# Kernel optimization log

Measured on AMD Instinct MI355X. Metric: run time of the kernel, lower is better.

The kernel has to match this reference:

```python
import jax, jax.numpy as jnp
import numpy as np

C = 192

def _dw_conv(x, w, k):
    # x: [B, C, H, W]; w: [C, 1, k, k]; depthwise => feature_group_count=C
    pad = k // 2
    return jax.lax.conv_general_dilated(
        x, w,
        window_strides=(1, 1),
        padding=[(pad, pad), (pad, pad)],
        dimension_numbers=("NCHW", "OIHW", "NCHW"),
        feature_group_count=x.shape[1],
    )

def setup_inputs() -> dict:
    key = jax.random.key(0)
    k1, k2, k3 = jax.random.split(key, 3)
    x = jax.random.normal(k1, (32, C, 64, 64), dtype=jnp.float32)
    # depthwise kernels: (out_ch=C, in_ch/groups=1, kh, kw), fan_in-style scaling
    w5 = jax.random.normal(k2, (C, 1, 5, 5), dtype=jnp.float32) * (1.0 / 5.0)
    w51 = jax.random.normal(k3, (C, 1, 51, 51), dtype=jnp.float32) * (1.0 / 51.0)
    return {"x": x, "w5": w5, "w51": w51}

def reference(x, w5, w51):
    # out = dw5(x) + dw51(x)
    return _dw_conv(x, w5, 5) + _dw_conv(x, w51, 51)
```

## Files before the change

### kernel.cpp

```cpp
#include <hip/hip_runtime.h>

typedef __bf16 bf16x8 __attribute__((ext_vector_type(8)));
typedef float  f32x16 __attribute__((ext_vector_type(16)));

__device__ __forceinline__ unsigned short f2bf_bits(float f) {
    unsigned int u = __builtin_bit_cast(unsigned int, f);
    u += 0x7FFFu + ((u >> 16) & 1u);
    return (unsigned short)(u >> 16);
}

__global__ void __launch_bounds__(256) dw5_51_kernel(
    const float* __restrict__ x,
    const float* __restrict__ w5,
    const float* __restrict__ w51,
    float* __restrict__ out)
{
    __shared__ unsigned short wlds[128 * 72];
    __shared__ unsigned short rowbuf[4][2][1088];

    const int tid = threadIdx.x;
    const int wg  = blockIdx.x;
    const int c   = wg >> 3;
    const int bg  = wg & 7;

    {
        const int s    = tid >> 1;
        const int half = tid & 1;
        const int kh   = 88 - s;
        const bool rowok = (kh >= 0) && (kh <= 50);
        #pragma unroll
        for (int j = 0; j < 32; ++j) {
            const int kw = half * 32 + j;
            float v = 0.0f;
            if (rowok && kw <= 50) {
                v = w51[c * 2601 + kh * 51 + kw];
                if (kh >= 23 && kh < 28 && kw >= 23 && kw < 28)
                    v += w5[c * 25 + (kh - 23) * 5 + (kw - 23)];
            }
            wlds[s * 72 + kw] = f2bf_bits(v);
        }
    }

    const int lane = tid & 63;
    const int wv   = tid >> 6;
    const int b    = bg * 4 + wv;
    const int n32  = lane & 31;
    const int gg   = lane >> 5;
    const int q    = lane & 7;
    const int u8   = n32 >> 3;

    {
        unsigned int* z = (unsigned int*)&rowbuf[wv][0][0];
        #pragma unroll
        for (int i = 0; i < 17; ++i) z[lane + 64 * i] = 0u;
    }
    __syncthreads();

    const long imgbase = ((long)b * 192 + c) * 4096;
    const float* xrow = x + imgbase + lane;
    float* outp = out + imgbase;

    const int bidx = 136 * q + 8 * u8 + 8 * gg;
    unsigned short* rb0 = &rowbuf[wv][0][0];
    unsigned short* rb1 = &rowbuf[wv][1][0];
    const int wbase = lane + 25;

    f32x16 acc00 = {}, acc01 = {}, acc10 = {}, acc11 = {};

    float xv = xrow[0];
    {
        const unsigned short xb = f2bf_bits(xv);
        #pragma unroll
        for (int qq = 0; qq < 8; ++qq) rb0[wbase + 135 * qq] = xb;
    }
    xv = xrow[64];

    #pragma unroll 1
    for (int rr = 0; rr < 64; rr += 2) {
        {
            const unsigned short xb = f2bf_bits(xv);
            #pragma unroll
            for (int qq = 0; qq < 8; ++qq) rb1[wbase + 135 * qq] = xb;
            if (rr + 2 < 64) xv = xrow[(rr + 2) * 64];

            bf16x8 Bf[4][2];
            #pragma unroll
            for (int ks = 0; ks < 4; ++ks) {
                Bf[ks][0] = *(const bf16x8*)&rb0[bidx + 16 * ks];
                Bf[ks][1] = *(const bf16x8*)&rb0[bidx + 16 * ks + 32];
            }
            if (rr <= 56) {
                const int srb = (63 - rr + n32) * 72 + 8 * gg;
                #pragma unroll
                for (int ks = 0; ks < 4; ++ks) {
                    const bf16x8 Af = *(const bf16x8*)&wlds[srb + 16 * ks];
                    acc00 = __builtin_amdgcn_mfma_f32_32x32x16_bf16(Af, Bf[ks][0], acc00, 0, 0, 0);
                    acc01 = __builtin_amdgcn_mfma_f32_32x32x16_bf16(Af, Bf[ks][1], acc01, 0, 0, 0);
                }
            }
            if (rr >= 7) {
                const int srb = (95 - rr + n32) * 72 + 8 * gg;
                #pragma unroll
                for (int ks = 0; ks < 4; ++ks) {
                    const bf16x8 Af = *(const bf16x8*)&wlds[srb + 16 * ks];
                    acc10 = __builtin_amdgcn_mfma_f32_32x32x16_bf16(Af, Bf[ks][0], acc10, 0, 0, 0);
                    acc11 = __builtin_amdgcn_mfma_f32_32x32x16_bf16(Af, Bf[ks][1], acc11, 0, 0, 0);
                }
            }
        }
        {
            const int r1 = rr + 1;
            if (rr + 2 < 64) {
                const unsigned short xb = f2bf_bits(xv);
                #pragma unroll
                for (int qq = 0; qq < 8; ++qq) rb0[wbase + 135 * qq] = xb;
                if (rr + 3 < 64) xv = xrow[(rr + 3) * 64];
            }
            bf16x8 Bf[4][2];
            #pragma unroll
            for (int ks = 0; ks < 4; ++ks) {
                Bf[ks][0] = *(const bf16x8*)&rb1[bidx + 16 * ks];
                Bf[ks][1] = *(const bf16x8*)&rb1[bidx + 16 * ks + 32];
            }
            if (r1 <= 56) {
                const int srb = (63 - r1 + n32) * 72 + 8 * gg;
                #pragma unroll
                for (int ks = 0; ks < 4; ++ks) {
                    const bf16x8 Af = *(const bf16x8*)&wlds[srb + 16 * ks];
                    acc00 = __builtin_amdgcn_mfma_f32_32x32x16_bf16(Af, Bf[ks][0], acc00, 0, 0, 0);
                    acc01 = __builtin_amdgcn_mfma_f32_32x32x16_bf16(Af, Bf[ks][1], acc01, 0, 0, 0);
                }
            }
            if (r1 >= 7) {
                const int srb = (95 - r1 + n32) * 72 + 8 * gg;
                #pragma unroll
                for (int ks = 0; ks < 4; ++ks) {
                    const bf16x8 Af = *(const bf16x8*)&wlds[srb + 16 * ks];
                    acc10 = __builtin_amdgcn_mfma_f32_32x32x16_bf16(Af, Bf[ks][0], acc10, 0, 0, 0);
                    acc11 = __builtin_amdgcn_mfma_f32_32x32x16_bf16(Af, Bf[ks][1], acc11, 0, 0, 0);
                }
            }
        }
    }

    #pragma unroll
    for (int v = 0; v < 16; ++v) {
        const int ho = (v & 3) + 8 * (v >> 2) + 4 * gg;
        outp[ho * 64 + n32]             = acc00[v];
        outp[ho * 64 + n32 + 32]        = acc01[v];
        outp[(ho + 32) * 64 + n32]      = acc10[v];
        outp[(ho + 32) * 64 + n32 + 32] = acc11[v];
    }
}

extern "C" void kernel_launch(void* const* d_in, const int* in_sizes, int n_in,
                              void* d_out, int out_size, void* d_ws, size_t ws_size,
                              hipStream_t stream) {
    (void)in_sizes; (void)n_in; (void)d_ws; (void)ws_size; (void)out_size;
    const float* x   = (const float*)d_in[0];
    const float* w5  = (const float*)d_in[1];
    const float* w51 = (const float*)d_in[2];
    float* out = (float*)d_out;
    dim3 grid(192 * 8), block(256);
    hipLaunchKernelGGL(dw5_51_kernel, grid, block, 0, stream, x, w5, w51, out);
}
```

Measured before the change: 148.7 us.

## Use 512-thread blocks with kw-chunked weight LDS layout and deduplicated B loads

Each workgroup now runs 8 waves covering 8 batch images per channel, which halves the number of times the 51x51 weight matrix is staged into LDS per channel. The weight LDS layout changes from row-padded (stride 72) to 8-column chunks of 1024 elements, so A-fragment reads become contiguous 16-byte loads that should avoid bank conflicts. The B fragments are loaded as 6 overlapping vectors instead of 8, because the two column halves share data. The larger block raises LDS use per workgroup and halves the grid, which may reduce occupancy or scheduling flexibility.

New measurement: 141.7 us. 4.7% less time.

```diff
diff --git a/kernel.cpp b/kernel.cpp
--- a/kernel.cpp
+++ b/kernel.cpp
@@ -9,41 +9,41 @@
     return (unsigned short)(u >> 16);
 }
 
-__global__ void __launch_bounds__(256) dw5_51_kernel(
+__global__ void __launch_bounds__(512) dw5_51_kernel(
     const float* __restrict__ x,
     const float* __restrict__ w5,
     const float* __restrict__ w51,
     float* __restrict__ out)
 {
-    __shared__ unsigned short wlds[128 * 72];
-    __shared__ unsigned short rowbuf[4][2][1088];
+    __shared__ unsigned short wlds[8 * 1024];
+    __shared__ unsigned short rowbuf[8][2][1088];
 
     const int tid = threadIdx.x;
     const int wg  = blockIdx.x;
-    const int c   = wg >> 3;
-    const int bg  = wg & 7;
+    const int c   = wg >> 2;
+    const int bg  = wg & 3;
 
     {
-        const int s    = tid >> 1;
-        const int half = tid & 1;
-        const int kh   = 88 - s;
+        const int s   = tid >> 2;
+        const int qtr = tid & 3;
+        const int kh  = 88 - s;
         const bool rowok = (kh >= 0) && (kh <= 50);
         #pragma unroll
-        for (int j = 0; j < 32; ++j) {
-            const int kw = half * 32 + j;
+        for (int i = 0; i < 16; ++i) {
+            const int kw = qtr * 16 + i;
             float v = 0.0f;
             if (rowok && kw <= 50) {
                 v = w51[c * 2601 + kh * 51 + kw];
                 if (kh >= 23 && kh < 28 && kw >= 23 && kw < 28)
                     v += w5[c * 25 + (kh - 23) * 5 + (kw - 23)];
             }
-            wlds[s * 72 + kw] = f2bf_bits(v);
+            wlds[(kw >> 3) * 1024 + s * 8 + (kw & 7)] = f2bf_bits(v);
         }
     }
 
     const int lane = tid & 63;
     const int wv   = tid >> 6;
-    const int b    = bg * 4 + wv;
+    const int b    = bg * 8 + wv;
     const int n32  = lane & 31;
     const int gg   = lane >> 5;
     const int q    = lane & 7;
@@ -67,6 +67,32 @@
 
     f32x16 acc00 = {}, acc01 = {}, acc10 = {}, acc11 = {};
 
+    const int abase = gg * 1024 + n32 * 8;
+
+    auto compute = [&](const unsigned short* __restrict__ rb, int r) {
+        bf16x8 d[6];
+        #pragma unroll
+        for (int t = 0; t < 6; ++t) d[t] = *(const bf16x8*)&rb[bidx + 16 * t];
+        if (r <= 56) {
+            const int ai = abase + (63 - r) * 8;
+            #pragma unroll
+            for (int ks = 0; ks < 4; ++ks) {
+                const bf16x8 Af = *(const bf16x8*)&wlds[ai + ks * 2048];
+                acc00 = __builtin_amdgcn_mfma_f32_32x32x16_bf16(Af, d[ks],     acc00, 0, 0, 0);
+                acc01 = __builtin_amdgcn_mfma_f32_32x32x16_bf16(Af, d[ks + 2], acc01, 0, 0, 0);
+            }
+        }
+        if (r >= 7) {
+            const int ai = abase + (95 - r) * 8;
+            #pragma unroll
+            for (int ks = 0; ks < 4; ++ks) {
+                const bf16x8 Af = *(const bf16x8*)&wlds[ai + ks * 2048];
+                acc10 = __builtin_amdgcn_mfma_f32_32x32x16_bf16(Af, d[ks],     acc10, 0, 0, 0);
+                acc11 = __builtin_amdgcn_mfma_f32_32x32x16_bf16(Af, d[ks + 2], acc11, 0, 0, 0);
+            }
+        }
+    };
+
     float xv = xrow[0];
     {
         const unsigned short xb = f2bf_bits(xv);
@@ -82,64 +108,16 @@
             #pragma unroll
             for (int qq = 0; qq < 8; ++qq) rb1[wbase + 135 * qq] = xb;
             if (rr + 2 < 64) xv = xrow[(rr + 2) * 64];
-
-            bf16x8 Bf[4][2];
-            #pragma unroll
-            for (int ks = 0; ks < 4; ++ks) {
-                Bf[ks][0] = *(const bf16x8*)&rb0[bidx + 16 * ks];
-                Bf[ks][1] = *(const bf16x8*)&rb0[bidx + 16 * ks + 32];
-            }
-            if (rr <= 56) {
-                const int srb = (63 - rr + n32) * 72 + 8 * gg;
-                #pragma unroll
-                for (int ks = 0; ks < 4; ++ks) {
-                    const bf16x8 Af = *(const bf16x8*)&wlds[srb + 16 * ks];
-                    acc00 = __builtin_amdgcn_mfma_f32_32x32x16_bf16(Af, Bf[ks][0], acc00, 0, 0, 0);
-                    acc01 = __builtin_amdgcn_mfma_f32_32x32x16_bf16(Af, Bf[ks][1], acc01, 0, 0, 0);
-                }
-            }
-            if (rr >= 7) {
-                const int srb = (95 - rr + n32) * 72 + 8 * gg;
-                #pragma unroll
-                for (int ks = 0; ks < 4; ++ks) {
-                    const bf16x8 Af = *(const bf16x8*)&wlds[srb + 16 * ks];
-                    acc10 = __builtin_amdgcn_mfma_f32_32x32x16_bf16(Af, Bf[ks][0], acc10, 0, 0, 0);
-                    acc11 = __builtin_amdgcn_mfma_f32_32x32x16_bf16(Af, Bf[ks][1], acc11, 0, 0, 0);
-                }
-            }
+            compute(rb0, rr);
         }
         {
-            const int r1 = rr + 1;
             if (rr + 2 < 64) {
                 const unsigned short xb = f2bf_bits(xv);
                 #pragma unroll
                 for (int qq = 0; qq < 8; ++qq) rb0[wbase + 135 * qq] = xb;
                 if (rr + 3 < 64) xv = xrow[(rr + 3) * 64];
             }
-            bf16x8 Bf[4][2];
-            #pragma unroll
-            for (int ks = 0; ks < 4; ++ks) {
-                Bf[ks][0] = *(const bf16x8*)&rb1[bidx + 16 * ks];
-                Bf[ks][1] = *(const bf16x8*)&rb1[bidx + 16 * ks + 32];
-            }
-            if (r1 <= 56) {
-                const int srb = (63 - r1 + n32) * 72 + 8 * gg;
-                #pragma unroll
-                for (int ks = 0; ks < 4; ++ks) {
-                    const bf16x8 Af = *(const bf16x8*)&wlds[srb + 16 * ks];
-                    acc00 = __builtin_amdgcn_mfma_f32_32x32x16_bf16(Af, Bf[ks][0], acc00, 0, 0, 0);
-                    acc01 = __builtin_amdgcn_mfma_f32_32x32x16_bf16(Af, Bf[ks][1], acc01, 0, 0, 0);
-                }
-            }
-            if (r1 >= 7) {
-                const int srb = (95 - r1 + n32) * 72 + 8 * gg;
-                #pragma unroll
-                for (int ks = 0; ks < 4; ++ks) {
-                    const bf16x8 Af = *(const bf16x8*)&wlds[srb + 16 * ks];
-                    acc10 = __builtin_amdgcn_mfma_f32_32x32x16_bf16(Af, Bf[ks][0], acc10, 0, 0, 0);
-                    acc11 = __builtin_amdgcn_mfma_f32_32x32x16_bf16(Af, Bf[ks][1], acc11, 0, 0, 0);
-                }
-            }
+            compute(rb1, rr + 1);
         }
     }
 
@@ -161,6 +139,6 @@
     const float* w5  = (const float*)d_in[1];
     const float* w51 = (const float*)d_in[2];
     float* out = (float*)d_out;
-    dim3 grid(192 * 8), block(256);
+    dim3 grid(192 * 4), block(512);
     hipLaunchKernelGGL(dw5_51_kernel, grid, block, 0, stream, x, w5, w51, out);
 }
```
